# Performance work log

Measured on AMD Instinct MI355X. Metric: run time of the kernel, lower is better.

## Reference

```python
import jax, jax.numpy as jnp
import numpy as np

B, T, D, H = 512, 1024, 12, 100


def setup_inputs() -> dict:
    key = jax.random.key(0)
    ks = jax.random.split(key, 5)
    x = jax.random.normal(ks[0], (B, T, D), dtype=jnp.float32)
    Wx = jax.random.normal(ks[1], (D, 4 * H), dtype=jnp.float32) * (1.0 / np.sqrt(D))
    Wh = jax.random.normal(ks[2], (H, 4 * H), dtype=jnp.float32) * (1.0 / np.sqrt(H))
    b = jnp.zeros((4 * H,), dtype=jnp.float32)
    Wd = jax.random.normal(ks[3], (H, D), dtype=jnp.float32) * (1.0 / np.sqrt(H))
    bd = jnp.zeros((D,), dtype=jnp.float32)
    return {"x": x, "Wx": Wx, "Wh": Wh, "b": b, "Wd": Wd, "bd": bd}


def _lstm_seq(x, Wx, Wh, b):
    # Precompute input projection for all timesteps (vectorized GEMM).
    xg = jnp.einsum('btd,dh->bth', x, Wx) + b  # [B, T, 4H]
    xg = jnp.transpose(xg, (1, 0, 2))          # [T, B, 4H] for scan

    def step(carry, xg_t):
        h, c = carry
        z = xg_t + h @ Wh                      # [B, 4H]
        i, f, g, o = jnp.split(z, 4, axis=-1)  # Keras gate order: i, f, c, o
        i = jax.nn.sigmoid(i)
        f = jax.nn.sigmoid(f)
        g = jnp.tanh(g)
        o = jax.nn.sigmoid(o)
        c = f * c + i * g
        h = o * jnp.tanh(c)
        return (h, c), h

    h0 = jnp.zeros((x.shape[0], Wh.shape[0]), dtype=x.dtype)
    c0 = jnp.zeros_like(h0)
    _, hs = jax.lax.scan(step, (h0, c0), xg)   # hs: [T, B, H]
    return jnp.transpose(hs, (1, 0, 2))        # [B, T, H]


def reference(x, Wx, Wh, b, Wd, bd):
    hs = _lstm_seq(x, Wx, Wh, b)               # [B, T, H]
    return jnp.einsum('bth,hd->btd', hs, Wd) + bd  # [B, T, 12]
```

## Files before the change

### kernel.cpp

```cpp
#include <hip/hip_runtime.h>
#include <math.h>

#define T_LEN 1024
#define BATCH 512
#define DIN   12
#define HID   100
#define G4    400
#define MB    4
#define NBLK  (BATCH / MB)
#define AROW  160
#define NW    8
#define NTHR  (NW * 64)
#define CHUNK 64
#define UNROLL 8

typedef _Float16 half8   __attribute__((ext_vector_type(8)));
typedef _Float16 half4_t __attribute__((ext_vector_type(4)));
typedef float    f32x4   __attribute__((ext_vector_type(4)));

static __device__ __forceinline__ float fast_exp2(float v) {
#if __has_builtin(__builtin_amdgcn_exp2f)
    return __builtin_amdgcn_exp2f(v);
#else
    return exp2f(v);
#endif
}
static __device__ __forceinline__ float fast_rcp(float v) {
#if __has_builtin(__builtin_amdgcn_rcpf)
    return __builtin_amdgcn_rcpf(v);
#else
    return 1.0f / v;
#endif
}

static __device__ __forceinline__ void wg_barrier_lds() {
    asm volatile("s_waitcnt lgkmcnt(0)\n\ts_barrier" ::: "memory");
}

__launch_bounds__(NTHR, 2)
__global__ void lstm_mfma_kernel(const float* __restrict__ x,
                                 const float* __restrict__ Wx,
                                 const float* __restrict__ Wh,
                                 const float* __restrict__ b,
                                 const float* __restrict__ Wd,
                                 const float* __restrict__ bd,
                                 float* __restrict__ out) {
    __shared__ __align__(16) char smem[65536];
    const int tid  = threadIdx.x;
    const int wid  = tid >> 6;
    const int lane = tid & 63;
    const int l    = lane & 15;
    const int quad = lane >> 4;
    const int b0   = blockIdx.x * MB;
    const int j    = wid * 16 + l;

    const float L2E = 1.4426950408889634f;

    _Float16* stage = (_Float16*)smem;
    half8 bfrag[4][4];
#pragma unroll
    for (int pass = 0; pass < 2; ++pass) {
#pragma unroll
        for (int gg = 0; gg < 2; ++gg) {
            const int G = pass * 2 + gg;
            const float gsc = (G == 2) ? (-2.f * L2E) : (-L2E);
#pragma unroll
            for (int kt = 0; kt < 4; ++kt) {
                half8 v;
#pragma unroll
                for (int jj = 0; jj < 8; ++jj) {
                    const int k = kt * 32 + quad * 8 + jj;
                    float w = 0.f;
                    if (wid < 7) {
                        if (j < HID) {
                            if (k < HID)            w = Wh[k * G4 + G * HID + j] * gsc;
                            else if (k < HID + DIN) w = Wx[(k - HID) * G4 + G * HID + j] * gsc;
                        }
                    } else if (G == 0) {
                        if (l < DIN && k < HID)     w = Wd[k * DIN + l];
                    }
                    v[jj] = (_Float16)w;
                }
                *(half8*)&stage[((wid * 8) + (gg * 4 + kt)) * 512 + lane * 8] = v;
            }
        }
        __syncthreads();
#pragma unroll
        for (int gg = 0; gg < 2; ++gg)
#pragma unroll
            for (int kt = 0; kt < 4; ++kt)
                bfrag[pass * 2 + gg][kt] =
                    *(half8*)&stage[((wid * 8) + (gg * 4 + kt)) * 512 + lane * 8];
        __syncthreads();
    }

    f32x4 biasC[4];
#pragma unroll
    for (int G = 0; G < 4; ++G) biasC[G] = (f32x4){0.f, 0.f, 0.f, 0.f};
    if (wid < 7) {
        if (j < HID) {
#pragma unroll
            for (int G = 0; G < 4; ++G) {
                const float gsc = (G == 2) ? (-2.f * L2E) : (-L2E);
                const float bv = b[G * HID + j] * gsc;
                biasC[G] = (f32x4){bv, bv, bv, bv};
            }
        }
    } else if (l < DIN) {
        const float bv = bd[l];
        biasC[0] = (f32x4){bv, bv, bv, bv};
    }

    _Float16 (*Ah)[MB][AROW] = (_Float16 (*)[MB][AROW])smem;
    _Float16* xchunk = (_Float16*)(smem + 2560);

    float4 pre0 = {0.f, 0.f, 0.f, 0.f}, pre1 = {0.f, 0.f, 0.f, 0.f};
    auto refill_load = [&](int c) {
        {
            const int f  = tid;
            const int m  = f / (CHUNK * DIN / 4);
            const int o  = f - m * (CHUNK * DIN / 4);
            const int tt = o / 3;
            const int dd = o - tt * 3;
            pre0 = *(const float4*)(x +
                ((size_t)(b0 + m) * T_LEN + c * CHUNK + tt) * DIN + dd * 4);
        }
        if (tid < (CHUNK * MB * DIN) / 4 - NTHR) {
            const int f  = tid + NTHR;
            const int m  = f / (CHUNK * DIN / 4);
            const int o  = f - m * (CHUNK * DIN / 4);
            const int tt = o / 3;
            const int dd = o - tt * 3;
            pre1 = *(const float4*)(x +
                ((size_t)(b0 + m) * T_LEN + c * CHUNK + tt) * DIN + dd * 4);
        }
    };
    auto refill_store = [&]() {
        {
            const int f  = tid;
            const int m  = f / (CHUNK * DIN / 4);
            const int o  = f - m * (CHUNK * DIN / 4);
            const int tt = o / 3;
            const int dd = o - tt * 3;
            half4_t h4;
            h4[0] = (_Float16)pre0.x; h4[1] = (_Float16)pre0.y;
            h4[2] = (_Float16)pre0.z; h4[3] = (_Float16)pre0.w;
            *(half4_t*)&xchunk[tt * (MB * DIN) + m * DIN + dd * 4] = h4;
        }
        if (tid < (CHUNK * MB * DIN) / 4 - NTHR) {
            const int f  = tid + NTHR;
            const int m  = f / (CHUNK * DIN / 4);
            const int o  = f - m * (CHUNK * DIN / 4);
            const int tt = o / 3;
            const int dd = o - tt * 3;
            half4_t h4;
            h4[0] = (_Float16)pre1.x; h4[1] = (_Float16)pre1.y;
            h4[2] = (_Float16)pre1.z; h4[3] = (_Float16)pre1.w;
            *(half4_t*)&xchunk[tt * (MB * DIN) + m * DIN + dd * 4] = h4;
        }
    };

    for (int i = tid; i < (2 * MB * AROW) / 2; i += NTHR) ((int*)smem)[i] = 0;
    refill_load(0);
    refill_store();
    __syncthreads();
    if (tid < MB * 3) {
        const int m = tid / 3, part = tid - (tid / 3) * 3;
        *(half4_t*)&Ah[0][m][HID + part * 4] =
            *(const half4_t*)&xchunk[m * DIN + part * 4];
    }
    __syncthreads();

    const bool gate_lane = (wid < 7) && (j < HID);
    const int  arow = l >> 2;

    float cs = 0.f;
    float obuf[UNROLL];

#pragma unroll 1
    for (int tb = 0; tb < T_LEN / UNROLL; ++tb) {
        const bool do_refill = (((tb + 1) & 7) == 0) && ((tb + 1) < T_LEN / UNROLL);
#pragma unroll
        for (int it = 0; it < UNROLL; ++it) {
            const int t  = tb * UNROLL + it;
            const int p  = it & 1;
            const int pn = p ^ 1;

            if (it == UNROLL - 2) {
                if (do_refill) refill_load((tb + 1) >> 3);
            }
            if (it == UNROLL - 1) {
                if (do_refill) {
                    refill_store();
                    wg_barrier_lds();
                }
            }

            half8 a[4];
#pragma unroll
            for (int kt = 0; kt < 4; ++kt)
                a[kt] = *(const half8*)&Ah[p][arow][kt * 32 + quad * 8];

            if (wid < 7) {
                f32x4 acc[4];
#pragma unroll
                for (int kt = 0; kt < 4; ++kt)
#pragma unroll
                    for (int Gi = 0; Gi < 4; ++Gi) {
                        constexpr int GO_[4] = {0, 2, 1, 3};
                        const int G = GO_[Gi];
                        acc[G] = __builtin_amdgcn_mfma_f32_16x16x32_f16(
                                     a[kt], bfrag[G][kt],
                                     (kt == 0) ? biasC[G] : acc[G], 0, 0, 0);
                    }

                if (gate_lane) {
                    const float ei = fast_exp2(acc[0][0]);
                    const float ef = fast_exp2(acc[1][0]);
                    const float eg = fast_exp2(acc[2][0]);
                    const float eo = fast_exp2(acc[3][0]);
                    const float gf  = fast_rcp(1.f + ef);
                    const float dd  = (1.f + ei) * (1.f + eg);
                    const float u   = __builtin_fmaf(eg, 2.f * L2E, -2.f * L2E);
                    const float gig = u * fast_rcp(dd);
                    cs = __builtin_fmaf(gf, cs, gig);
                    const float ec = fast_exp2(cs);
                    const float hv = (1.f - ec) * fast_rcp((1.f + eo) * (1.f + ec));
                    Ah[pn][quad][j] = (_Float16)hv;
                }
            } else {
                if ((t + 1) < T_LEN && lane < MB * 3) {
                    const int m = lane / 3, part = lane - (lane / 3) * 3;
                    *(half4_t*)&Ah[pn][m][HID + part * 4] =
                        *(const half4_t*)&xchunk[((t + 1) & (CHUNK - 1)) * (MB * DIN)
                                                 + m * DIN + part * 4];
                }
                f32x4 accP;
#pragma unroll
                for (int kt = 0; kt < 4; ++kt)
                    accP = __builtin_amdgcn_mfma_f32_16x16x32_f16(
                               a[kt], bfrag[0][kt],
                               (kt == 0) ? biasC[0] : accP, 0, 0, 0);
                obuf[it] = accP[0];
            }
            wg_barrier_lds();
        }
        if (wid == 7 && l < DIN) {
#pragma unroll
            for (int s = 0; s < UNROLL; ++s) {
                const int row = tb * UNROLL + s - 1;
                if (row >= 0)
                    out[((size_t)(b0 + quad) * T_LEN + row) * DIN + l] = obuf[s];
            }
        }
    }

    if (wid == 7) {
        half8 a[4];
#pragma unroll
        for (int kt = 0; kt < 4; ++kt)
            a[kt] = *(const half8*)&Ah[0][arow][kt * 32 + quad * 8];
        f32x4 accP;
#pragma unroll
        for (int kt = 0; kt < 4; ++kt)
            accP = __builtin_amdgcn_mfma_f32_16x16x32_f16(
                       a[kt], bfrag[0][kt],
                       (kt == 0) ? biasC[0] : accP, 0, 0, 0);
        if (l < DIN)
            out[((size_t)(b0 + quad) * T_LEN + (T_LEN - 1)) * DIN + l] = accP[0];
    }
}

extern "C" void kernel_launch(void* const* d_in, const int* in_sizes, int n_in,
                              void* d_out, int out_size, void* d_ws, size_t ws_size,
                              hipStream_t stream) {
    const float* x  = (const float*)d_in[0];
    const float* Wx = (const float*)d_in[1];
    const float* Wh = (const float*)d_in[2];
    const float* b  = (const float*)d_in[3];
    const float* Wd = (const float*)d_in[4];
    const float* bd = (const float*)d_in[5];
    float* out = (float*)d_out;

    lstm_mfma_kernel<<<NBLK, NTHR, 0, stream>>>(x, Wx, Wh, b, Wd, bd, out);
}
```

Measured before the change: 530.8 us.

## Fold output projection into spare columns of last gate wave, drop eighth wave

The workgroup shrinks from 8 to 7 waves. The 12 output-projection columns and the x staging move into the unused columns of wave 6, whose gate columns 96-99 leave 12 lanes free. Every wave now runs the same MFMA path with no divergent branch, and the per-step barrier synchronises fewer waves. The cost is that wave 6 does the gate math, the projection stores and the x staging together, which lengthens its critical path, and the column-index remapping must line up exactly.

```diff
diff --git a/kernel.cpp b/kernel.cpp
--- a/kernel.cpp
+++ b/kernel.cpp
@@ -9,7 +9,7 @@
 #define MB    4
 #define NBLK  (BATCH / MB)
 #define AROW  160
-#define NW    8
+#define NW    7
 #define NTHR  (NW * 64)
 #define CHUNK 64
 #define UNROLL 8
@@ -71,13 +71,13 @@
                 for (int jj = 0; jj < 8; ++jj) {
                     const int k = kt * 32 + quad * 8 + jj;
                     float w = 0.f;
-                    if (wid < 7) {
+                    if (wid < 6 || l < 4) {
                         if (j < HID) {
                             if (k < HID)            w = Wh[k * G4 + G * HID + j] * gsc;
                             else if (k < HID + DIN) w = Wx[(k - HID) * G4 + G * HID + j] * gsc;
                         }
                     } else if (G == 0) {
-                        if (l < DIN && k < HID)     w = Wd[k * DIN + l];
+                        if (k < HID)                w = Wd[k * DIN + (l - 4)];
                     }
                     v[jj] = (_Float16)w;
                 }
@@ -97,7 +97,7 @@
     f32x4 biasC[4];
 #pragma unroll
     for (int G = 0; G < 4; ++G) biasC[G] = (f32x4){0.f, 0.f, 0.f, 0.f};
-    if (wid < 7) {
+    if (wid < 6 || l < 4) {
         if (j < HID) {
 #pragma unroll
             for (int G = 0; G < 4; ++G) {
@@ -106,8 +106,8 @@
                 biasC[G] = (f32x4){bv, bv, bv, bv};
             }
         }
-    } else if (l < DIN) {
-        const float bv = bd[l];
+    } else {
+        const float bv = bd[l - 4];
         biasC[0] = (f32x4){bv, bv, bv, bv};
     }
 
@@ -171,7 +171,9 @@
     }
     __syncthreads();
 
-    const bool gate_lane = (wid < 7) && (j < HID);
+    const bool gate_lane = (j < HID);
+    const bool proj_lane = (wid == 6) && (l >= 4);
+    const bool stag_lane = (wid == 6) && (lane >= 20) && (lane < 32);
     const int  arow = l >> 2;
 
     float cs = 0.f;
@@ -201,61 +203,56 @@
             for (int kt = 0; kt < 4; ++kt)
                 a[kt] = *(const half8*)&Ah[p][arow][kt * 32 + quad * 8];
 
-            if (wid < 7) {
-                f32x4 acc[4];
-#pragma unroll
-                for (int kt = 0; kt < 4; ++kt)
-#pragma unroll
-                    for (int Gi = 0; Gi < 4; ++Gi) {
-                        constexpr int GO_[4] = {0, 2, 1, 3};
-                        const int G = GO_[Gi];
-                        acc[G] = __builtin_amdgcn_mfma_f32_16x16x32_f16(
-                                     a[kt], bfrag[G][kt],
-                                     (kt == 0) ? biasC[G] : acc[G], 0, 0, 0);
-                    }
-
-                if (gate_lane) {
-                    const float ei = fast_exp2(acc[0][0]);
-                    const float ef = fast_exp2(acc[1][0]);
-                    const float eg = fast_exp2(acc[2][0]);
-                    const float eo = fast_exp2(acc[3][0]);
-                    const float gf  = fast_rcp(1.f + ef);
-                    const float dd  = (1.f + ei) * (1.f + eg);
-                    const float u   = __builtin_fmaf(eg, 2.f * L2E, -2.f * L2E);
-                    const float gig = u * fast_rcp(dd);
-                    cs = __builtin_fmaf(gf, cs, gig);
-                    const float ec = fast_exp2(cs);
-                    const float hv = (1.f - ec) * fast_rcp((1.f + eo) * (1.f + ec));
-                    Ah[pn][quad][j] = (_Float16)hv;
+            if (stag_lane && (t + 1) < T_LEN) {
+                const int idx = lane - 20;
+                const int m = idx / 3, part = idx - (idx / 3) * 3;
+                *(half4_t*)&Ah[pn][m][HID + part * 4] =
+                    *(const half4_t*)&xchunk[((t + 1) & (CHUNK - 1)) * (MB * DIN)
+                                             + m * DIN + part * 4];
+            }
+
+            f32x4 acc[4];
+#pragma unroll
+            for (int kt = 0; kt < 4; ++kt)
+#pragma unroll
+                for (int Gi = 0; Gi < 4; ++Gi) {
+                    constexpr int GO_[4] = {0, 2, 1, 3};
+                    const int G = GO_[Gi];
+                    acc[G] = __builtin_amdgcn_mfma_f32_16x16x32_f16(
+                                 a[kt], bfrag[G][kt],
+                                 (kt == 0) ? biasC[G] : acc[G], 0, 0, 0);
                 }
-            } else {
-                if ((t + 1) < T_LEN && lane < MB * 3) {
-                    const int m = lane / 3, part = lane - (lane / 3) * 3;
-                    *(half4_t*)&Ah[pn][m][HID + part * 4] =
-                        *(const half4_t*)&xchunk[((t + 1) & (CHUNK - 1)) * (MB * DIN)
-                                                 + m * DIN + part * 4];
-                }
-                f32x4 accP;
-#pragma unroll
-                for (int kt = 0; kt < 4; ++kt)
-                    accP = __builtin_amdgcn_mfma_f32_16x16x32_f16(
-                               a[kt], bfrag[0][kt],
-                               (kt == 0) ? biasC[0] : accP, 0, 0, 0);
-                obuf[it] = accP[0];
-            }
+
+            if (gate_lane) {
+                const float ei = fast_exp2(acc[0][0]);
+                const float ef = fast_exp2(acc[1][0]);
+                const float eg = fast_exp2(acc[2][0]);
+                const float eo = fast_exp2(acc[3][0]);
+                const float gf  = fast_rcp(1.f + ef);
+                const float dd  = (1.f + ei) * (1.f + eg);
+                const float u   = __builtin_fmaf(eg, 2.f * L2E, -2.f * L2E);
+                const float gig = u * fast_rcp(dd);
+                cs = __builtin_fmaf(gf, cs, gig);
+                const float ec = fast_exp2(cs);
+                const float hv = (1.f - ec) * fast_rcp((1.f + eo) * (1.f + ec));
+                Ah[pn][quad][j] = (_Float16)hv;
+            }
+            if (proj_lane)
+                obuf[it] = acc[0][0];
+
             wg_barrier_lds();
         }
-        if (wid == 7 && l < DIN) {
+        if (proj_lane) {
 #pragma unroll
             for (int s = 0; s < UNROLL; ++s) {
                 const int row = tb * UNROLL + s - 1;
                 if (row >= 0)
-                    out[((size_t)(b0 + quad) * T_LEN + row) * DIN + l] = obuf[s];
-            }
-        }
-    }
-
-    if (wid == 7) {
+                    out[((size_t)(b0 + quad) * T_LEN + row) * DIN + (l - 4)] = obuf[s];
+            }
+        }
+    }
+
+    if (wid == 6) {
         half8 a[4];
 #pragma unroll
         for (int kt = 0; kt < 4; ++kt)
@@ -266,8 +263,8 @@
             accP = __builtin_amdgcn_mfma_f32_16x16x32_f16(
                        a[kt], bfrag[0][kt],
                        (kt == 0) ? biasC[0] : accP, 0, 0, 0);
-        if (l < DIN)
-            out[((size_t)(b0 + quad) * T_LEN + (T_LEN - 1)) * DIN + l] = accP[0];
+        if (l >= 4)
+            out[((size_t)(b0 + quad) * T_LEN + (T_LEN - 1)) * DIN + (l - 4)] = accP[0];
     }
 }
 
```

Measured after the change: 527.3 us. About the same (-0.7%).
